# Performance work log

Hardware: AMD Instinct MI355X
Metric: run time of the kernel (lower is better)

## Reference

```python
import jax, jax.numpy as jnp
import numpy as np

N_NODES, N_EDGES, D, H, L = 50000, 1000000, 64, 4, 4
C = D // H
NEG_SLOPE = 0.2


def _layernorm(x, w, b, eps=1e-5):
    mu = x.mean(-1, keepdims=True)
    var = ((x - mu) ** 2).mean(-1, keepdims=True)
    return (x - mu) * jax.lax.rsqrt(var + eps) * w + b


def setup_inputs() -> dict:
    key = jax.random.key(0)
    ks = jax.random.split(key, 12)
    s = 0.2  # weight scale to keep activations well-conditioned
    return {
        "node_feats": jax.random.normal(ks[0], (N_NODES, D), jnp.float32),
        "edge_feats": jax.random.normal(ks[1], (N_EDGES, D), jnp.float32),
        "edge_index": jax.random.randint(ks[2], (2, N_EDGES), 0, N_NODES, jnp.int32),
        "gat_lin_w": jax.random.normal(ks[3], (L, D, D), jnp.float32) * s,
        "gat_lin_edge_w": jax.random.normal(ks[4], (L, D, D), jnp.float32) * s,
        "gat_att_src": jax.random.normal(ks[5], (L, H, C), jnp.float32) * s,
        "gat_att_dst": jax.random.normal(ks[6], (L, H, C), jnp.float32) * s,
        "gat_att_edge": jax.random.normal(ks[7], (L, H, C), jnp.float32) * s,
        "gat_bias": jnp.zeros((L, D), jnp.float32),
        "ln_w": jnp.ones((L, D), jnp.float32),
        "ln_b": jnp.zeros((L, D), jnp.float32),
        "eu_w1": jax.random.normal(ks[8], (L, 3 * D, 3 * D), jnp.float32) * s,
        "eu_b1": jnp.zeros((L, 3 * D), jnp.float32),
        "eu_ln_w": jnp.ones((L, 3 * D), jnp.float32),
        "eu_ln_b": jnp.zeros((L, 3 * D), jnp.float32),
        "eu_w2": jax.random.normal(ks[9], (L, 3 * D, D), jnp.float32) * s,
        "eu_b2": jnp.zeros((L, D), jnp.float32),
    }


def _gat_forward(node_feats, edge_feats, edge_index,
                 gat_lin_w, gat_lin_edge_w, gat_att_src, gat_att_dst,
                 gat_att_edge, gat_bias, ln_w, ln_b,
                 eu_w1, eu_b1, eu_ln_w, eu_ln_b, eu_w2, eu_b2):
    N = node_feats.shape[0]
    loop = jnp.arange(N, dtype=edge_index.dtype)
    # add self loops once (topology fixed); self-loop edge attr = zeros
    ei_sl = jnp.concatenate([edge_index, jnp.stack([loop, loop])], axis=1)
    src, dst = ei_sl[0], ei_sl[1]
    e_src, e_dst = edge_index[0], edge_index[1]

    for l in range(L):
        e_sl = jnp.concatenate(
            [edge_feats, jnp.zeros((N, D), edge_feats.dtype)], axis=0)
        xh = (node_feats @ gat_lin_w[l]).reshape(N, H, C)          # [N,H,C]
        a_src = (xh * gat_att_src[l]).sum(-1)                      # [N,H]
        a_dst = (xh * gat_att_dst[l]).sum(-1)                      # [N,H]
        eh = (e_sl @ gat_lin_edge_w[l]).reshape(-1, H, C)          # [E+N,H,C]
        a_edge = (eh * gat_att_edge[l]).sum(-1)                    # [E+N,H]

        alpha = jax.nn.leaky_relu(a_src[src] + a_dst[dst] + a_edge, NEG_SLOPE)
        amax = jax.ops.segment_max(alpha, dst, num_segments=N)     # every node has a self loop
        ex = jnp.exp(alpha - amax[dst])
        denom = jax.ops.segment_sum(ex, dst, num_segments=N)
        coef = ex / (denom[dst] + 1e-16)                           # [E+N,H]

        msg = xh[src] * coef[:, :, None]                           # [E+N,H,C]
        out = jax.ops.segment_sum(msg, dst, num_segments=N).reshape(N, D)
        out = out + gat_bias[l]
        out = _layernorm(out, ln_w[l], ln_b[l])
        h = out if l == L - 1 else jax.nn.relu(out)
        node_feats = h + node_feats                                # residual (dropout=eval/identity)

        # sparse edge update: gather -> MLP -> residual
        z = jnp.concatenate(
            [node_feats[e_src], node_feats[e_dst], edge_feats], axis=-1)
        z = _layernorm(z @ eu_w1[l] + eu_b1[l], eu_ln_w[l], eu_ln_b[l])
        z = jax.nn.relu(z)
        edge_feats = z @ eu_w2[l] + eu_b2[l] + edge_feats

    return node_feats, edge_feats


def reference(node_feats, edge_feats, edge_index, gat_lin_w, gat_lin_edge_w,
              gat_att_src, gat_att_dst, gat_att_edge, gat_bias, ln_w, ln_b,
              eu_w1, eu_b1, eu_ln_w, eu_ln_b, eu_w2, eu_b2):
    return _gat_forward(node_feats, edge_feats, edge_index,
                        gat_lin_w, gat_lin_edge_w, gat_att_src, gat_att_dst,
                        gat_att_edge, gat_bias, ln_w, ln_b,
                        eu_w1, eu_b1, eu_ln_w, eu_ln_b, eu_w2, eu_b2)
```

## Files before the change

kernel.cpp:

```cpp
#include <hip/hip_runtime.h>
#include <hip/hip_bf16.h>

#define NN 50000
#define NE 1000000
#define DD 64
#define HH 4
#define LL 4
#define D3 192
#define NT (NE + NN)

typedef float f32x4 __attribute__((ext_vector_type(4)));
typedef short bf16x8 __attribute__((ext_vector_type(8)));

__device__ __forceinline__ unsigned short f2bf(float f){
    union { __hip_bfloat16 b; unsigned short u; } cv;
    cv.b = __float2bfloat16(f);
    return cv.u;
}
__device__ __forceinline__ float bf2f(unsigned short u){
    return __uint_as_float(((unsigned)u) << 16);
}
__device__ __forceinline__ unsigned pk2(float a, float b){
    union { __hip_bfloat162 v; unsigned u; } cv;
    cv.v = __float22bfloat162_rn(float2{a, b});
    return cv.u;
}
__device__ __forceinline__ float lrelu(float x){ return x > 0.f ? x : 0.2f * x; }

__global__ __launch_bounds__(256) void k_hist(const int* __restrict__ ei, int* __restrict__ deg){
    for (int e = blockIdx.x * 256 + threadIdx.x; e < NE; e += gridDim.x * 256)
        atomicAdd(&deg[ei[NE + e]], 1);
}

__global__ __launch_bounds__(1024) void k_scan(const int* __restrict__ deg,
                                               int* __restrict__ row,
                                               int* __restrict__ cursor){
    __shared__ int sm[1024];
    __shared__ int carry_s;
    int t = threadIdx.x;
    if (t == 0) carry_s = 0;
    __syncthreads();
    for (int base = 0; base < NN; base += 1024) {
        int i = base + t;
        int v = (i < NN) ? deg[i] + 1 : 0;
        sm[t] = v;
        __syncthreads();
        for (int off = 1; off < 1024; off <<= 1) {
            int x = (t >= off) ? sm[t - off] : 0;
            __syncthreads();
            sm[t] += x;
            __syncthreads();
        }
        int incl = sm[t];
        int carry = carry_s;
        if (i < NN) {
            int excl = carry + incl - v;
            row[i] = excl;
            cursor[i] = excl;
        }
        __syncthreads();
        if (t == 1023) carry_s = carry + incl;
        __syncthreads();
    }
    if (t == 0) row[NN] = carry_s;
}

__global__ __launch_bounds__(256) void k_scatter(const int* __restrict__ ei,
                                                 int* __restrict__ cursor,
                                                 int* __restrict__ pos,
                                                 int* __restrict__ srcs){
    for (int e = blockIdx.x * 256 + threadIdx.x; e < NE; e += gridDim.x * 256) {
        int d = ei[NE + e];
        int j = atomicAdd(&cursor[d], 1);
        pos[e] = j;
        srcs[j] = ei[e];
    }
}

__global__ __launch_bounds__(256) void k_self(const int* __restrict__ row,
                                              int* __restrict__ srcs){
    int n = blockIdx.x * 256 + threadIdx.x;
    if (n < NN) srcs[row[n + 1] - 1] = n;
}

__global__ __launch_bounds__(256) void k_prepall(const float* __restrict__ w1,
                                                 const float* __restrict__ w2,
                                                 const float* __restrict__ we,
                                                 const float* __restrict__ atte,
                                                 unsigned short* __restrict__ w1f_all,
                                                 unsigned short* __restrict__ w2f_all,
                                                 float* __restrict__ V_all){
    int l = blockIdx.x / 194;
    int i = (blockIdx.x % 194) * 256 + threadIdx.x;
    unsigned short* w1f = w1f_all + (size_t)l * D3 * D3;
    unsigned short* w2f = w2f_all + (size_t)l * DD * D3;
    float* V = V_all + l * DD * HH;
    if (i < 36864) {
        int c = i / 3072, r = i % 3072;
        int kc = r / 512, r2 = r % 512;
        int lane = r2 >> 3, m = r2 & 7;
        int k = kc * 32 + (lane >> 4) * 8 + m;
        int n = c * 16 + (lane & 15);
        w1f[i] = f2bf(w1[(size_t)l * D3 * D3 + k * D3 + n]);
    } else if (i < 49152) {
        int j = i - 36864;
        int c = j / 3072, r = j % 3072;
        int kc = r / 512, r2 = r % 512;
        int lane = r2 >> 3, m = r2 & 7;
        int k = kc * 32 + (lane >> 4) * 8 + m;
        int n = c * 16 + (lane & 15);
        w2f[j] = f2bf(w2[(size_t)l * D3 * DD + k * DD + n]);
    } else if (i < 49152 + DD * HH) {
        int j = i - 49152;
        int k = j >> 2, h = j & 3;
        float s = 0.f;
        #pragma unroll
        for (int c = 0; c < 16; c++)
            s += we[(size_t)l * DD * DD + k * DD + h * 16 + c] * atte[l * DD + h * 16 + c];
        V[j] = s;
    }
}

__global__ __launch_bounds__(256) void k_aedge(const float* __restrict__ ef,
                                               const int* __restrict__ pos,
                                               const float* __restrict__ Vg,
                                               float* __restrict__ aedge_s){
    __shared__ float Vl[256];
    Vl[threadIdx.x] = Vg[threadIdx.x];
    __syncthreads();
    int gk = threadIdx.x & 7;
    int em = threadIdx.x >> 3;
    int c0 = gk * 8;
    for (int eb = blockIdx.x * 32; eb < NE; eb += gridDim.x * 32) {
        int e = eb + em;
        const float4* ep = (const float4*)(ef + (size_t)e * 64 + c0);
        float4 v0 = ep[0];
        float4 v1 = ep[1];
        float p0, p1, p2, p3;
        {
            const float* Vp = &Vl[c0 * 4];
            p0 = v0.x*Vp[0] + v0.y*Vp[4] + v0.z*Vp[8]  + v0.w*Vp[12]
               + v1.x*Vp[16] + v1.y*Vp[20] + v1.z*Vp[24] + v1.w*Vp[28];
            p1 = v0.x*Vp[1] + v0.y*Vp[5] + v0.z*Vp[9]  + v0.w*Vp[13]
               + v1.x*Vp[17] + v1.y*Vp[21] + v1.z*Vp[25] + v1.w*Vp[29];
            p2 = v0.x*Vp[2] + v0.y*Vp[6] + v0.z*Vp[10] + v0.w*Vp[14]
               + v1.x*Vp[18] + v1.y*Vp[22] + v1.z*Vp[26] + v1.w*Vp[30];
            p3 = v0.x*Vp[3] + v0.y*Vp[7] + v0.z*Vp[11] + v0.w*Vp[15]
               + v1.x*Vp[19] + v1.y*Vp[23] + v1.z*Vp[27] + v1.w*Vp[31];
        }
        #pragma unroll
        for (int m = 1; m < 8; m <<= 1) {
            p0 += __shfl_xor(p0, m);
            p1 += __shfl_xor(p1, m);
            p2 += __shfl_xor(p2, m);
            p3 += __shfl_xor(p3, m);
        }
        if (gk == 0) {
            int j = pos[e];
            float4 ae = {p0, p1, p2, p3};
            *(float4*)(aedge_s + (size_t)j * 4) = ae;
        }
    }
}

__global__ __launch_bounds__(256) void k_nodelin(const float* __restrict__ x,
                                                 const float* __restrict__ Wg,
                                                 const float* __restrict__ attsrc,
                                                 const float* __restrict__ attdst,
                                                 unsigned short* __restrict__ xh,
                                                 float* __restrict__ a_src,
                                                 float* __restrict__ a_dst, int l){
    __shared__ float Wl[64 * 64];
    __shared__ float xr[4 * 64];
    int t = threadIdx.x;
    const float* W = Wg + (size_t)l * 4096;
    for (int i = t; i < 4096; i += 256) Wl[i] = W[i];
    int row = blockIdx.x * 4 + (t >> 6);
    int col = t & 63;
    if (row < NN) xr[t] = x[(size_t)row * 64 + col];
    __syncthreads();
    float acc = 0.f;
    const float* xp = &xr[(t >> 6) * 64];
    #pragma unroll
    for (int k = 0; k < 64; k++) acc += xp[k] * Wl[k * 64 + col];
    float ps = acc * attsrc[l * 64 + col];
    float pd = acc * attdst[l * 64 + col];
    #pragma unroll
    for (int m = 1; m < 16; m <<= 1) { ps += __shfl_xor(ps, m); pd += __shfl_xor(pd, m); }
    if (row < NN) {
        xh[(size_t)row * 64 + col] = f2bf(acc);
        if ((col & 15) == 0) {
            a_src[row * 4 + (col >> 4)] = ps;
            a_dst[row * 4 + (col >> 4)] = pd;
        }
    }
}

__global__ __launch_bounds__(256) void k_attnfused(const int* __restrict__ row,
                                                   const int* __restrict__ srcs,
                                                   float* __restrict__ aedge_s,
                                                   const float* __restrict__ a_src,
                                                   const float* __restrict__ a_dst,
                                                   const unsigned short* __restrict__ xh,
                                                   const float* __restrict__ bias,
                                                   const float* __restrict__ lnw,
                                                   const float* __restrict__ lnb,
                                                   const float* __restrict__ xcur,
                                                   float* __restrict__ xnext,
                                                   unsigned short* __restrict__ xbf,
                                                   int l, int dorelu){
    int n = blockIdx.x * 4 + (threadIdx.x >> 6);
    if (n >= NN) return;
    int lane = threadIdx.x & 63;
    int a = row[n], b = row[n + 1];
    int len = b - a;

    const float4 ad = *(const float4*)(a_dst + (size_t)n * 4);
    float4 mx = {-1e30f, -1e30f, -1e30f, -1e30f};
    float4 sum = {0.f, 0.f, 0.f, 0.f};

    if (len <= 64) {
        int j = a + lane;
        bool act = lane < len;
        float4 val = {-1e30f, -1e30f, -1e30f, -1e30f};
        if (act) {
            int s = srcs[j];
            const float4 as = *(const float4*)(a_src + (size_t)s * 4);
            const float4 ae = *(const float4*)(aedge_s + (size_t)j * 4);
            val.x = lrelu(as.x + ad.x + ae.x);
            val.y = lrelu(as.y + ad.y + ae.y);
            val.z = lrelu(as.z + ad.z + ae.z);
            val.w = lrelu(as.w + ad.w + ae.w);
        }
        mx = val;
        #pragma unroll
        for (int m = 1; m < 64; m <<= 1) {
            mx.x = fmaxf(mx.x, __shfl_xor(mx.x, m));
            mx.y = fmaxf(mx.y, __shfl_xor(mx.y, m));
            mx.z = fmaxf(mx.z, __shfl_xor(mx.z, m));
            mx.w = fmaxf(mx.w, __shfl_xor(mx.w, m));
        }
        float4 ex = {0.f, 0.f, 0.f, 0.f};
        if (act) {
            ex.x = expf(val.x - mx.x);
            ex.y = expf(val.y - mx.y);
            ex.z = expf(val.z - mx.z);
            ex.w = expf(val.w - mx.w);
            *(float4*)(aedge_s + (size_t)j * 4) = ex;
        }
        sum = ex;
        #pragma unroll
        for (int m = 1; m < 64; m <<= 1) {
            sum.x += __shfl_xor(sum.x, m);
            sum.y += __shfl_xor(sum.y, m);
            sum.z += __shfl_xor(sum.z, m);
            sum.w += __shfl_xor(sum.w, m);
        }
    } else {
        for (int j0 = a; j0 < b; j0 += 64) {
            int j = j0 + lane;
            if (j < b) {
                int s = srcs[j];
                const float4 as = *(const float4*)(a_src + (size_t)s * 4);
                const float4 ae = *(const float4*)(aedge_s + (size_t)j * 4);
                mx.x = fmaxf(mx.x, lrelu(as.x + ad.x + ae.x));
                mx.y = fmaxf(mx.y, lrelu(as.y + ad.y + ae.y));
                mx.z = fmaxf(mx.z, lrelu(as.z + ad.z + ae.z));
                mx.w = fmaxf(mx.w, lrelu(as.w + ad.w + ae.w));
            }
        }
        #pragma unroll
        for (int m = 1; m < 64; m <<= 1) {
            mx.x = fmaxf(mx.x, __shfl_xor(mx.x, m));
            mx.y = fmaxf(mx.y, __shfl_xor(mx.y, m));
            mx.z = fmaxf(mx.z, __shfl_xor(mx.z, m));
            mx.w = fmaxf(mx.w, __shfl_xor(mx.w, m));
        }
        for (int j0 = a; j0 < b; j0 += 64) {
            int j = j0 + lane;
            if (j < b) {
                int s = srcs[j];
                const float4 as = *(const float4*)(a_src + (size_t)s * 4);
                const float4 ae = *(const float4*)(aedge_s + (size_t)j * 4);
                float4 ex;
                ex.x = expf(lrelu(as.x + ad.x + ae.x) - mx.x);
                ex.y = expf(lrelu(as.y + ad.y + ae.y) - mx.y);
                ex.z = expf(lrelu(as.z + ad.z + ae.z) - mx.z);
                ex.w = expf(lrelu(as.w + ad.w + ae.w) - mx.w);
                *(float4*)(aedge_s + (size_t)j * 4) = ex;
                sum.x += ex.x; sum.y += ex.y; sum.z += ex.z; sum.w += ex.w;
            }
        }
        #pragma unroll
        for (int m = 1; m < 64; m <<= 1) {
            sum.x += __shfl_xor(sum.x, m);
            sum.y += __shfl_xor(sum.y, m);
            sum.z += __shfl_xor(sum.z, m);
            sum.w += __shfl_xor(sum.w, m);
        }
    }

    int h = lane >> 4;
    float sumh = (h == 0) ? sum.x : (h == 1) ? sum.y : (h == 2) ? sum.z : sum.w;
    float invh = 1.f / (sumh + 1e-16f);

    float accv = 0.f;
    #pragma unroll 8
    for (int j = a; j < b; ++j) {
        int s = srcs[j];
        float coef = aedge_s[(size_t)j * 4 + h] * invh;
        accv = fmaf(bf2f(xh[(size_t)s * 64 + lane]), coef, accv);
    }

    if (lane < 4) aedge_s[(size_t)(b - 1) * 4 + lane] = 0.f;

    float v = accv + bias[l * 64 + lane];
    float s = v, q = v * v;
    #pragma unroll
    for (int m = 1; m < 64; m <<= 1) { s += __shfl_xor(s, m); q += __shfl_xor(q, m); }
    float mu = s * (1.f / 64.f);
    float var = q * (1.f / 64.f) - mu * mu;
    float y = (v - mu) * rsqrtf(var + 1e-5f) * lnw[l * 64 + lane] + lnb[l * 64 + lane];
    if (dorelu) y = fmaxf(y, 0.f);
    float out = y + xcur[(size_t)n * 64 + lane];
    xnext[(size_t)n * 64 + lane] = out;
    xbf[(size_t)n * 64 + lane] = f2bf(out);
}

#define ET 64
__global__ __launch_bounds__(256, 4) void k_edgemlp(const unsigned short* __restrict__ xbf,
                                                    const float* __restrict__ ein,
                                                    float* __restrict__ eout,
                                                    const int* __restrict__ ei,
                                                    const unsigned short* __restrict__ w1f,
                                                    const unsigned short* __restrict__ w2f,
                                                    const float* __restrict__ b1g,
                                                    const float* __restrict__ lnwg,
                                                    const float* __restrict__ lnbg,
                                                    const float* __restrict__ b2g, int l){
    __shared__ __align__(16) unsigned short zin[ET * 192];
    __shared__ float red[ET][2][2];
    __shared__ float eres[ET][68];

    int t = threadIdx.x;
    int base = blockIdx.x * ET;

    int wid = t >> 6, lane = t & 63;

    {
        int ge = base + lane;
        int sidx = ei[ge], didx = ei[NE + ge];
        #pragma unroll
        for (int i = 0; i < 6; i++) {
            int g = i * 4 + wid;
            uint4 wv;
            if (g < 16) {
                const unsigned short* srcb = (g < 8)
                    ? (xbf + (size_t)sidx * 64 + g * 8)
                    : (xbf + (size_t)didx * 64 + (g - 8) * 8);
                wv = *(const uint4*)srcb;
            } else {
                const float* src = ein + (size_t)ge * 64 + (g - 16) * 8;
                float4 v0 = *(const float4*)src;
                float4 v1 = *(const float4*)(src + 4);
                int c0 = (g - 16) * 8;
                eres[lane][c0 + 0] = v0.x; eres[lane][c0 + 1] = v0.y;
                eres[lane][c0 + 2] = v0.z; eres[lane][c0 + 3] = v0.w;
                eres[lane][c0 + 4] = v1.x; eres[lane][c0 + 5] = v1.y;
                eres[lane][c0 + 6] = v1.z; eres[lane][c0 + 7] = v1.w;
                wv.x = pk2(v0.x, v0.y); wv.y = pk2(v0.z, v0.w);
                wv.z = pk2(v1.x, v1.y); wv.w = pk2(v1.z, v1.w);
            }
            *(uint4*)&zin[lane * 192 + ((g ^ (lane & 7)) << 3)] = wv;
        }
    }
    __syncthreads();

    int wr = wid >> 1, wc = wid & 1;
    int l15 = lane & 15, l4 = lane >> 4;
    int eb = wr * 32;

    f32x4 zz = {0.f, 0.f, 0.f, 0.f};
    f32x4 acc[2][6];
    #pragma unroll
    for (int mt = 0; mt < 2; mt++)
        #pragma unroll
        for (int nt = 0; nt < 6; nt++) acc[mt][nt] = zz;

    #pragma unroll
    for (int kc = 0; kc < 6; kc++) {
        int ko = kc * 32 + l4 * 8;
        int gg = ko >> 3;
        bf16x8 af[2], bfv[6];
        #pragma unroll
        for (int mt = 0; mt < 2; mt++) {
            int row = eb + mt * 16 + l15;
            af[mt] = *(const bf16x8*)&zin[row * 192 + ((gg ^ (row & 7)) << 3)];
        }
        #pragma unroll
        for (int nt = 0; nt < 6; nt++)
            bfv[nt] = *(const bf16x8*)&w1f[(size_t)(((wc * 6 + nt) * 6 + kc) << 9) + (lane << 3)];
        #pragma unroll
        for (int mt = 0; mt < 2; mt++)
            #pragma unroll
            for (int nt = 0; nt < 6; nt++)
                acc[mt][nt] = __builtin_amdgcn_mfma_f32_16x16x32_bf16(af[mt], bfv[nt], acc[mt][nt], 0, 0, 0);
    }

    float b1v[6], lnwv[6], lnbv[6];
    #pragma unroll
    for (int nt = 0; nt < 6; nt++) {
        int col = wc * 96 + nt * 16 + l15;
        b1v[nt] = b1g[l * D3 + col];
        lnwv[nt] = lnwg[l * D3 + col];
        lnbv[nt] = lnbg[l * D3 + col];
    }
    float ps[2][4], pq[2][4];
    #pragma unroll
    for (int mt = 0; mt < 2; mt++)
        #pragma unroll
        for (int r = 0; r < 4; r++) {
            float s = 0.f, q = 0.f;
            #pragma unroll
            for (int nt = 0; nt < 6; nt++) {
                float v = acc[mt][nt][r] + b1v[nt];
                acc[mt][nt][r] = v;
                s += v; q += v * v;
            }
            #pragma unroll
            for (int m = 1; m < 16; m <<= 1) { s += __shfl_xor(s, m); q += __shfl_xor(q, m); }
            ps[mt][r] = s; pq[mt][r] = q;
        }
    if (l15 == 0) {
        #pragma unroll
        for (int mt = 0; mt < 2; mt++)
            #pragma unroll
            for (int r = 0; r < 4; r++) {
                int er = eb + mt * 16 + l4 * 4 + r;
                red[er][wc][0] = ps[mt][r];
                red[er][wc][1] = pq[mt][r];
            }
    }
    __syncthreads();

    #pragma unroll
    for (int mt = 0; mt < 2; mt++)
        #pragma unroll
        for (int r = 0; r < 4; r++) {
            int er = eb + mt * 16 + l4 * 4 + r;
            float s = red[er][0][0] + red[er][1][0];
            float q = red[er][0][1] + red[er][1][1];
            float mu = s * (1.f / 192.f);
            float rs = rsqrtf(q * (1.f / 192.f) - mu * mu + 1e-5f);
            #pragma unroll
            for (int nt = 0; nt < 6; nt++) {
                float v = (acc[mt][nt][r] - mu) * rs * lnwv[nt] + lnbv[nt];
                v = fmaxf(v, 0.f);
                int col = wc * 96 + nt * 16 + l15;
                int gg = col >> 3;
                zin[er * 192 + ((gg ^ (er & 7)) << 3) + (col & 7)] = f2bf(v);
            }
        }
    __syncthreads();

    f32x4 a2[4];
    a2[0] = zz; a2[1] = zz; a2[2] = zz; a2[3] = zz;
    #pragma unroll
    for (int kc = 0; kc < 6; kc++) {
        int ko = kc * 32 + l4 * 8;
        int gg = ko >> 3;
        int row = wid * 16 + l15;
        bf16x8 af = *(const bf16x8*)&zin[row * 192 + ((gg ^ (row & 7)) << 3)];
        #pragma unroll
        for (int nt = 0; nt < 4; nt++) {
            bf16x8 bg = *(const bf16x8*)&w2f[(size_t)((nt * 6 + kc) << 9) + (lane << 3)];
            a2[nt] = __builtin_amdgcn_mfma_f32_16x16x32_bf16(af, bg, a2[nt], 0, 0, 0);
        }
    }
    int eb2 = wid * 16;
    #pragma unroll
    for (int r = 0; r < 4; r++) {
        int er = eb2 + l4 * 4 + r;
        size_t ge = (size_t)base + er;
        #pragma unroll
        for (int nt = 0; nt < 4; nt++) {
            int col = nt * 16 + l15;
            float v = a2[nt][r] + b2g[l * 64 + col] + eres[er][col];
            eout[ge * 64 + col] = v;
        }
    }
}

extern "C" void kernel_launch(void* const* d_in, const int* in_sizes, int n_in,
                              void* d_out, int out_size, void* d_ws, size_t ws_size,
                              hipStream_t stream) {
    (void)in_sizes; (void)n_in; (void)out_size; (void)ws_size;
    const float* node_in = (const float*)d_in[0];
    const float* edge_in = (const float*)d_in[1];
    const int*   ei      = (const int*)d_in[2];
    const float* gat_lin_w = (const float*)d_in[3];
    const float* gat_lin_edge_w = (const float*)d_in[4];
    const float* att_src = (const float*)d_in[5];
    const float* att_dst = (const float*)d_in[6];
    const float* att_edge = (const float*)d_in[7];
    const float* gat_bias = (const float*)d_in[8];
    const float* ln_w = (const float*)d_in[9];
    const float* ln_b = (const float*)d_in[10];
    const float* eu_w1 = (const float*)d_in[11];
    const float* eu_b1 = (const float*)d_in[12];
    const float* eu_ln_w = (const float*)d_in[13];
    const float* eu_ln_b = (const float*)d_in[14];
    const float* eu_w2 = (const float*)d_in[15];
    const float* eu_b2 = (const float*)d_in[16];

    float* out_node = (float*)d_out;
    float* out_edge = out_node + (size_t)NN * DD;

    float* ws = (float*)d_ws;
    unsigned short* xh = (unsigned short*)ws; ws += (size_t)(NN * DD) / 2;
    unsigned short* xbf = (unsigned short*)ws; ws += (size_t)(NN * DD) / 2;
    float* a_src = ws; ws += (size_t)NN * HH;
    float* a_dst = ws; ws += (size_t)NN * HH;
    float* node_a = ws; ws += (size_t)NN * DD;
    float* node_b = ws; ws += (size_t)NN * DD;
    unsigned short* w1f_all = (unsigned short*)ws; ws += (LL * D3 * D3) / 2;
    unsigned short* w2f_all = (unsigned short*)ws; ws += (LL * DD * D3) / 2;
    float* V_all = ws; ws += LL * DD * HH;
    int* deg    = (int*)ws; ws += NN;
    int* cursor = (int*)ws; ws += NN;
    int* row    = (int*)ws; ws += NN + 4;
    int* pos    = (int*)ws; ws += NE;
    int* srcs   = (int*)ws; ws += NT;
    float* aedge_s = ws; ws += (size_t)NT * HH;

    hipMemsetAsync(deg, 0, NN * sizeof(int), stream);
    hipMemsetAsync(aedge_s, 0, (size_t)NT * HH * sizeof(float), stream);
    k_hist<<<2048, 256, 0, stream>>>(ei, deg);
    k_scan<<<1, 1024, 0, stream>>>(deg, row, cursor);
    k_scatter<<<2048, 256, 0, stream>>>(ei, cursor, pos, srcs);
    k_self<<<(NN + 255) / 256, 256, 0, stream>>>(row, srcs);
    k_prepall<<<LL * 194, 256, 0, stream>>>(eu_w1, eu_w2, gat_lin_edge_w, att_edge,
                                            w1f_all, w2f_all, V_all);

    for (int l = 0; l < LL; l++) {
        const float* ncur = (l == 0) ? node_in : ((l == 1) ? node_a : ((l == 2) ? node_b : node_a));
        float* nnext = (l == 0) ? node_a : ((l == 1) ? node_b : ((l == 2) ? node_a : out_node));
        const float* ecur = (l == 0) ? edge_in : out_edge;

        k_aedge<<<4096, 256, 0, stream>>>(ecur, pos, V_all + l * DD * HH, aedge_s);
        k_nodelin<<<12500, 256, 0, stream>>>(ncur, gat_lin_w, att_src, att_dst, xh, a_src, a_dst, l);
        k_attnfused<<<12500, 256, 0, stream>>>(row, srcs, aedge_s, a_src, a_dst, xh,
                                               gat_bias, ln_w, ln_b, ncur, nnext, xbf,
                                               l, (l < LL - 1) ? 1 : 0);
        k_edgemlp<<<NE / ET, 256, 0, stream>>>(xbf, ecur, out_edge, ei,
                                               w1f_all + (size_t)l * D3 * D3,
                                               w2f_all + (size_t)l * DD * D3,
                                               eu_b1, eu_ln_w, eu_ln_b, eu_b2, l);
    }
}
```

Baseline: 2.077 ms.

## Make edge MLP kernel persistent with register prefetch of next edge tile

```diff
diff --git a/kernel.cpp b/kernel.cpp
--- a/kernel.cpp
+++ b/kernel.cpp
@@ -328,7 +328,8 @@
 }
 
 #define ET 64
-__global__ __launch_bounds__(256, 4) void k_edgemlp(const unsigned short* __restrict__ xbf,
+#define EGRID 2048
+__global__ __launch_bounds__(256, 2) void k_edgemlp(const unsigned short* __restrict__ xbf,
                                                     const float* __restrict__ ein,
                                                     float* __restrict__ eout,
                                                     const int* __restrict__ ei,
@@ -342,70 +343,13 @@
     __shared__ float red[ET][2][2];
     __shared__ float eres[ET][68];
 
+    const int ntiles = NE / ET;
     int t = threadIdx.x;
-    int base = blockIdx.x * ET;
-
     int wid = t >> 6, lane = t & 63;
-
-    {
-        int ge = base + lane;
-        int sidx = ei[ge], didx = ei[NE + ge];
-        #pragma unroll
-        for (int i = 0; i < 6; i++) {
-            int g = i * 4 + wid;
-            uint4 wv;
-            if (g < 16) {
-                const unsigned short* srcb = (g < 8)
-                    ? (xbf + (size_t)sidx * 64 + g * 8)
-                    : (xbf + (size_t)didx * 64 + (g - 8) * 8);
-                wv = *(const uint4*)srcb;
-            } else {
-                const float* src = ein + (size_t)ge * 64 + (g - 16) * 8;
-                float4 v0 = *(const float4*)src;
-                float4 v1 = *(const float4*)(src + 4);
-                int c0 = (g - 16) * 8;
-                eres[lane][c0 + 0] = v0.x; eres[lane][c0 + 1] = v0.y;
-                eres[lane][c0 + 2] = v0.z; eres[lane][c0 + 3] = v0.w;
-                eres[lane][c0 + 4] = v1.x; eres[lane][c0 + 5] = v1.y;
-                eres[lane][c0 + 6] = v1.z; eres[lane][c0 + 7] = v1.w;
-                wv.x = pk2(v0.x, v0.y); wv.y = pk2(v0.z, v0.w);
-                wv.z = pk2(v1.x, v1.y); wv.w = pk2(v1.z, v1.w);
-            }
-            *(uint4*)&zin[lane * 192 + ((g ^ (lane & 7)) << 3)] = wv;
-        }
-    }
-    __syncthreads();
-
     int wr = wid >> 1, wc = wid & 1;
     int l15 = lane & 15, l4 = lane >> 4;
     int eb = wr * 32;
-
-    f32x4 zz = {0.f, 0.f, 0.f, 0.f};
-    f32x4 acc[2][6];
-    #pragma unroll
-    for (int mt = 0; mt < 2; mt++)
-        #pragma unroll
-        for (int nt = 0; nt < 6; nt++) acc[mt][nt] = zz;
-
-    #pragma unroll
-    for (int kc = 0; kc < 6; kc++) {
-        int ko = kc * 32 + l4 * 8;
-        int gg = ko >> 3;
-        bf16x8 af[2], bfv[6];
-        #pragma unroll
-        for (int mt = 0; mt < 2; mt++) {
-            int row = eb + mt * 16 + l15;
-            af[mt] = *(const bf16x8*)&zin[row * 192 + ((gg ^ (row & 7)) << 3)];
-        }
-        #pragma unroll
-        for (int nt = 0; nt < 6; nt++)
-            bfv[nt] = *(const bf16x8*)&w1f[(size_t)(((wc * 6 + nt) * 6 + kc) << 9) + (lane << 3)];
-        #pragma unroll
-        for (int mt = 0; mt < 2; mt++)
-            #pragma unroll
-            for (int nt = 0; nt < 6; nt++)
-                acc[mt][nt] = __builtin_amdgcn_mfma_f32_16x16x32_bf16(af[mt], bfv[nt], acc[mt][nt], 0, 0, 0);
-    }
+    int swz = lane & 7;
 
     float b1v[6], lnwv[6], lnbv[6];
     #pragma unroll
@@ -415,80 +359,167 @@
         lnwv[nt] = lnwg[l * D3 + col];
         lnbv[nt] = lnbg[l * D3 + col];
     }
-    float ps[2][4], pq[2][4];
+    float b2v[4];
     #pragma unroll
-    for (int mt = 0; mt < 2; mt++)
-        #pragma unroll
-        for (int r = 0; r < 4; r++) {
-            float s = 0.f, q = 0.f;
-            #pragma unroll
-            for (int nt = 0; nt < 6; nt++) {
-                float v = acc[mt][nt][r] + b1v[nt];
-                acc[mt][nt][r] = v;
-                s += v; q += v * v;
-            }
-            #pragma unroll
-            for (int m = 1; m < 16; m <<= 1) { s += __shfl_xor(s, m); q += __shfl_xor(q, m); }
-            ps[mt][r] = s; pq[mt][r] = q;
-        }
-    if (l15 == 0) {
+    for (int nt = 0; nt < 4; nt++) b2v[nt] = b2g[l * 64 + nt * 16 + l15];
+
+    uint4 rx0, rx1, rx2, rx3;
+    float4 re0a, re0b, re1a, re1b;
+
+#define LOAD_TILE(T)                                                       \
+    {                                                                      \
+        int ge_ = (T) * ET + lane;                                         \
+        int sidx_ = ei[ge_], didx_ = ei[NE + ge_];                         \
+        const unsigned short* xs_ = xbf + (size_t)sidx_ * 64;              \
+        const unsigned short* xd_ = xbf + (size_t)didx_ * 64;              \
+        rx0 = *(const uint4*)(xs_ + wid * 8);                              \
+        rx1 = *(const uint4*)(xs_ + (wid + 4) * 8);                        \
+        rx2 = *(const uint4*)(xd_ + wid * 8);                              \
+        rx3 = *(const uint4*)(xd_ + (wid + 4) * 8);                        \
+        const float* ep_ = ein + (size_t)ge_ * 64;                         \
+        re0a = *(const float4*)(ep_ + wid * 8);                            \
+        re0b = *(const float4*)(ep_ + wid * 8 + 4);                        \
+        re1a = *(const float4*)(ep_ + (wid + 4) * 8);                      \
+        re1b = *(const float4*)(ep_ + (wid + 4) * 8 + 4);                  \
+    }
+
+    int tile = blockIdx.x;
+    if (tile >= ntiles) return;
+    LOAD_TILE(tile);
+
+    for (; tile < ntiles; tile += EGRID) {
+        int base = tile * ET;
+        *(uint4*)&zin[lane * 192 + (((wid)      ^ swz) << 3)] = rx0;
+        *(uint4*)&zin[lane * 192 + (((wid + 4)  ^ swz) << 3)] = rx1;
+        *(uint4*)&zin[lane * 192 + (((wid + 8)  ^ swz) << 3)] = rx2;
+        *(uint4*)&zin[lane * 192 + (((wid + 12) ^ swz) << 3)] = rx3;
+        {
+            uint4 w;
+            w.x = pk2(re0a.x, re0a.y); w.y = pk2(re0a.z, re0a.w);
+            w.z = pk2(re0b.x, re0b.y); w.w = pk2(re0b.z, re0b.w);
+            *(uint4*)&zin[lane * 192 + (((wid + 16) ^ swz) << 3)] = w;
+            int c0 = wid * 8;
+            eres[lane][c0 + 0] = re0a.x; eres[lane][c0 + 1] = re0a.y;
+            eres[lane][c0 + 2] = re0a.z; eres[lane][c0 + 3] = re0a.w;
+            eres[lane][c0 + 4] = re0b.x; eres[lane][c0 + 5] = re0b.y;
+            eres[lane][c0 + 6] = re0b.z; eres[lane][c0 + 7] = re0b.w;
+            w.x = pk2(re1a.x, re1a.y); w.y = pk2(re1a.z, re1a.w);
+            w.z = pk2(re1b.x, re1b.y); w.w = pk2(re1b.z, re1b.w);
+            *(uint4*)&zin[lane * 192 + (((wid + 20) ^ swz) << 3)] = w;
+            c0 = (wid + 4) * 8;
+            eres[lane][c0 + 0] = re1a.x; eres[lane][c0 + 1] = re1a.y;
+            eres[lane][c0 + 2] = re1a.z; eres[lane][c0 + 3] = re1a.w;
+            eres[lane][c0 + 4] = re1b.x; eres[lane][c0 + 5] = re1b.y;
+            eres[lane][c0 + 6] = re1b.z; eres[lane][c0 + 7] = re1b.w;
+        }
+        {
+            int tn = tile + EGRID;
+            if (tn < ntiles) LOAD_TILE(tn);
+        }
+        __syncthreads();
+
+        f32x4 zz = {0.f, 0.f, 0.f, 0.f};
+        f32x4 acc[2][6];
+        #pragma unroll
+        for (int mt = 0; mt < 2; mt++)
+            #pragma unroll
+            for (int nt = 0; nt < 6; nt++) acc[mt][nt] = zz;
+
+        #pragma unroll
+        for (int kc = 0; kc < 6; kc++) {
+            int gg = kc * 4 + l4;
+            bf16x8 af[2], bfv[6];
+            #pragma unroll
+            for (int mt = 0; mt < 2; mt++) {
+                int row = eb + mt * 16 + l15;
+                af[mt] = *(const bf16x8*)&zin[row * 192 + ((gg ^ (row & 7)) << 3)];
+            }
+            #pragma unroll
+            for (int nt = 0; nt < 6; nt++)
+                bfv[nt] = *(const bf16x8*)&w1f[(size_t)(((wc * 6 + nt) * 6 + kc) << 9) + (lane << 3)];
+            #pragma unroll
+            for (int mt = 0; mt < 2; mt++)
+                #pragma unroll
+                for (int nt = 0; nt < 6; nt++)
+                    acc[mt][nt] = __builtin_amdgcn_mfma_f32_16x16x32_bf16(af[mt], bfv[nt], acc[mt][nt], 0, 0, 0);
+        }
+
+        float ps[2][4], pq[2][4];
+        #pragma unroll
+        for (int mt = 0; mt < 2; mt++)
+            #pragma unroll
+            for (int r = 0; r < 4; r++) {
+                float s = 0.f, q = 0.f;
+                #pragma unroll
+                for (int nt = 0; nt < 6; nt++) {
+                    float v = acc[mt][nt][r] + b1v[nt];
+                    acc[mt][nt][r] = v;
+                    s += v; q += v * v;
+                }
+                #pragma unroll
+                for (int m = 1; m < 16; m <<= 1) { s += __shfl_xor(s, m); q += __shfl_xor(q, m); }
+                ps[mt][r] = s; pq[mt][r] = q;
+            }
+        if (l15 == 0) {
+            #pragma unroll
+            for (int mt = 0; mt < 2; mt++)
+                #pragma unroll
+                for (int r = 0; r < 4; r++) {
+                    int er = eb + mt * 16 + l4 * 4 + r;
+                    red[er][wc][0] = ps[mt][r];
+                    red[er][wc][1] = pq[mt][r];
+                }
+        }
+        __syncthreads();
+
         #pragma unroll
         for (int mt = 0; mt < 2; mt++)
             #pragma unroll
             for (int r = 0; r < 4; r++) {
                 int er = eb + mt * 16 + l4 * 4 + r;
-                red[er][wc][0] = ps[mt][r];
-                red[er][wc][1] = pq[mt][r];
-            }
-    }
-    __syncthreads();
-
-    #pragma unroll
-    for (int mt = 0; mt < 2; mt++)
+                float s = red[er][0][0] + red[er][1][0];
+                float q = red[er][0][1] + red[er][1][1];
+                float mu = s * (1.f / 192.f);
+                float rs = rsqrtf(q * (1.f / 192.f) - mu * mu + 1e-5f);
+                #pragma unroll
+                for (int nt = 0; nt < 6; nt++) {
+                    float v = (acc[mt][nt][r] - mu) * rs * lnwv[nt] + lnbv[nt];
+                    v = fmaxf(v, 0.f);
+                    int col = wc * 96 + nt * 16 + l15;
+                    int gg = col >> 3;
+                    zin[er * 192 + ((gg ^ (er & 7)) << 3) + (col & 7)] = f2bf(v);
+                }
+            }
+        __syncthreads();
+
+        f32x4 a2[4];
+        a2[0] = zz; a2[1] = zz; a2[2] = zz; a2[3] = zz;
+        #pragma unroll
+        for (int kc = 0; kc < 6; kc++) {
+            int gg = kc * 4 + l4;
+            int row = wid * 16 + l15;
+            bf16x8 af = *(const bf16x8*)&zin[row * 192 + ((gg ^ (row & 7)) << 3)];
+            #pragma unroll
+            for (int nt = 0; nt < 4; nt++) {
+                bf16x8 bg = *(const bf16x8*)&w2f[(size_t)((nt * 6 + kc) << 9) + (lane << 3)];
+                a2[nt] = __builtin_amdgcn_mfma_f32_16x16x32_bf16(af, bg, a2[nt], 0, 0, 0);
+            }
+        }
+        int eb2 = wid * 16;
         #pragma unroll
         for (int r = 0; r < 4; r++) {
-            int er = eb + mt * 16 + l4 * 4 + r;
-            float s = red[er][0][0] + red[er][1][0];
-            float q = red[er][0][1] + red[er][1][1];
-            float mu = s * (1.f / 192.f);
-            float rs = rsqrtf(q * (1.f / 192.f) - mu * mu + 1e-5f);
-            #pragma unroll
-            for (int nt = 0; nt < 6; nt++) {
-                float v = (acc[mt][nt][r] - mu) * rs * lnwv[nt] + lnbv[nt];
-                v = fmaxf(v, 0.f);
-                int col = wc * 96 + nt * 16 + l15;
-                int gg = col >> 3;
-                zin[er * 192 + ((gg ^ (er & 7)) << 3) + (col & 7)] = f2bf(v);
-            }
-        }
-    __syncthreads();
-
-    f32x4 a2[4];
-    a2[0] = zz; a2[1] = zz; a2[2] = zz; a2[3] = zz;
-    #pragma unroll
-    for (int kc = 0; kc < 6; kc++) {
-        int ko = kc * 32 + l4 * 8;
-        int gg = ko >> 3;
-        int row = wid * 16 + l15;
-        bf16x8 af = *(const bf16x8*)&zin[row * 192 + ((gg ^ (row & 7)) << 3)];
-        #pragma unroll
-        for (int nt = 0; nt < 4; nt++) {
-            bf16x8 bg = *(const bf16x8*)&w2f[(size_t)((nt * 6 + kc) << 9) + (lane << 3)];
-            a2[nt] = __builtin_amdgcn_mfma_f32_16x16x32_bf16(af, bg, a2[nt], 0, 0, 0);
-        }
-    }
-    int eb2 = wid * 16;
-    #pragma unroll
-    for (int r = 0; r < 4; r++) {
-        int er = eb2 + l4 * 4 + r;
-        size_t ge = (size_t)base + er;
-        #pragma unroll
-        for (int nt = 0; nt < 4; nt++) {
-            int col = nt * 16 + l15;
-            float v = a2[nt][r] + b2g[l * 64 + col] + eres[er][col];
-            eout[ge * 64 + col] = v;
-        }
-    }
+            int er = eb2 + l4 * 4 + r;
+            size_t ge = (size_t)base + er;
+            #pragma unroll
+            for (int nt = 0; nt < 4; nt++) {
+                int col = nt * 16 + l15;
+                float v = a2[nt][r] + b2v[nt] + eres[er][col];
+                eout[ge * 64 + col] = v;
+            }
+        }
+        __syncthreads();
+    }
+#undef LOAD_TILE
 }
 
 extern "C" void kernel_launch(void* const* d_in, const int* in_sizes, int n_in,
@@ -552,9 +583,9 @@
         k_attnfused<<<12500, 256, 0, stream>>>(row, srcs, aedge_s, a_src, a_dst, xh,
                                                gat_bias, ln_w, ln_b, ncur, nnext, xbf,
                                                l, (l < LL - 1) ? 1 : 0);
-        k_edgemlp<<<NE / ET, 256, 0, stream>>>(xbf, ecur, out_edge, ei,
-                                               w1f_all + (size_t)l * D3 * D3,
-                                               w2f_all + (size_t)l * DD * D3,
-                                               eu_b1, eu_ln_w, eu_ln_b, eu_b2, l);
-    }
-}
+        k_edgemlp<<<EGRID, 256, 0, stream>>>(xbf, ecur, out_edge, ei,
+                                             w1f_all + (size_t)l * D3 * D3,
+                                             w2f_all + (size_t)l * DD * D3,
+                                             eu_b1, eu_ln_w, eu_ln_b, eu_b2, l);
+    }
+}
```

Measured after the change: 5.687 ms. 174% more time.
